# Optimization experiments

Measured on AMD Instinct MI355X. Metric: run time of the kernel, lower is better.

## Reference

```python
import jax, jax.numpy as jnp
import numpy as np

B, N, D = 2, 2048, 2048
H = 16
HD = D // H  # 128


def setup_inputs() -> dict:
    key = jax.random.key(0)
    k1, k2, k3 = jax.random.split(key, 3)
    x = jax.random.normal(k1, (B, N, D), dtype=jnp.float32)
    # Linear weights stored as [in, out] so y = x @ W matches torch's x @ W.T
    Wq = jax.random.normal(k2, (D, D), dtype=jnp.float32) * (D ** -0.5)
    Wo = jax.random.normal(k3, (D, D), dtype=jnp.float32) * (D ** -0.5)
    bo = jnp.zeros((D,), dtype=jnp.float32)
    return {"x": x, "Wq": Wq, "Wo": Wo, "bo": bo}


def reference(x, Wq, Wo, bo):
    # NOTE: source module (faithfully) projects q, k, v all with q_matrix.
    b, n, d = x.shape
    q = x @ Wq                                   # [B, N, D]
    qh = q.reshape(b, n, H, HD).transpose(0, 2, 1, 3)  # [B, H, N, HD]
    scores = jnp.einsum("bhnd,bhmd->bhnm", qh, qh) * (HD ** -0.5)  # [B,H,N,N]
    attn = jax.nn.softmax(scores, axis=-1)
    y = jnp.einsum("bhnm,bhmd->bhnd", attn, qh)  # [B, H, N, HD]
    y = y.transpose(0, 2, 1, 3).reshape(b, n, d)  # [B, N, D]
    return y @ Wo + bo
```

## Files before the change

### kernel.cpp

```cpp
#include <hip/hip_runtime.h>
#include <hip/hip_bf16.h>

#define BATCH 2
#define SEQ   2048
#define DIM   2048
#define NHEAD 16
#define HDIM  128

#define KSTRIDE 136
#define VSTRIDE 72
#define PSTRIDE 72

typedef __bf16 bf16;
typedef __attribute__((ext_vector_type(2))) __bf16 bf16x2;
typedef __attribute__((ext_vector_type(4))) __bf16 bf16x4;
typedef __attribute__((ext_vector_type(8))) __bf16 bf16x8;
typedef __attribute__((ext_vector_type(4))) float f32x4;

__device__ __forceinline__ void load_lds16(const bf16* g, bf16* l) {
    __builtin_amdgcn_global_load_lds((const __attribute__((address_space(1))) void*)g,
                                     (__attribute__((address_space(3))) void*)l, 16, 0, 0);
}

__device__ __forceinline__ float exp2_hw(float x) { return __builtin_amdgcn_exp2f(x); }

__global__ __launch_bounds__(256)
void prep_kernel(const float* __restrict__ x, bf16* __restrict__ xb,
                 const float* __restrict__ Wq, bf16* __restrict__ Wtq,
                 const float* __restrict__ Wo, bf16* __restrict__ Wto)
{
    __shared__ bf16 T[64 * 72];
    const int bid = blockIdx.x;
    if (bid < 4096) {
        const size_t i = ((size_t)bid * 256 + threadIdx.x) * 8;
        const float4 f0 = *(const float4*)(x + i);
        const float4 f1 = *(const float4*)(x + i + 4);
        *(bf16x8*)(xb + i) = (bf16x8){(bf16)f0.x, (bf16)f0.y, (bf16)f0.z, (bf16)f0.w,
                                      (bf16)f1.x, (bf16)f1.y, (bf16)f1.z, (bf16)f1.w};
        return;
    }
    int t = bid - 4096;
    const float* W  = (t < 1024) ? Wq : Wo;
    bf16*        Wt = (t < 1024) ? Wtq : Wto;
    t &= 1023;
    const int kb = (t >> 5) * 64, nb = (t & 31) * 64;

    const int a = threadIdx.x & 31;
    const int g = threadIdx.x >> 5;
    {
        const float* s0 = W + (size_t)(kb + 2 * a) * DIM + nb + g * 8;
        const float4 r0a = *(const float4*)(s0);
        const float4 r0b = *(const float4*)(s0 + 4);
        const float4 r1a = *(const float4*)(s0 + DIM);
        const float4 r1b = *(const float4*)(s0 + DIM + 4);
        float v0[8] = {r0a.x, r0a.y, r0a.z, r0a.w, r0b.x, r0b.y, r0b.z, r0b.w};
        float v1[8] = {r1a.x, r1a.y, r1a.z, r1a.w, r1b.x, r1b.y, r1b.z, r1b.w};
        #pragma unroll
        for (int i = 0; i < 8; ++i)
            *(bf16x2*)&T[(g * 8 + i) * 72 + 2 * a] = (bf16x2){(bf16)v0[i], (bf16)v1[i]};
    }
    __syncthreads();

    const int r  = threadIdx.x >> 2;
    const int k0 = (threadIdx.x & 3) * 16;
    bf16x8 o0 = *(const bf16x8*)&T[r * 72 + k0];
    bf16x8 o1 = *(const bf16x8*)&T[r * 72 + k0 + 8];
    *(bf16x8*)(Wt + (size_t)(nb + r) * DIM + kb + k0)     = o0;
    *(bf16x8*)(Wt + (size_t)(nb + r) * DIM + kb + k0 + 8) = o1;
}

template<bool OUT_F32_BIAS>
__global__ __launch_bounds__(256)
void gemm_bt(const bf16* __restrict__ A, const bf16* __restrict__ Bt,
             const float* __restrict__ bias, void* __restrict__ Cptr,
             int M, int N, int K)
{
    __shared__ bf16 As[2][128 * 32];
    __shared__ bf16 Bs[2][128 * 32];

    const int tid  = threadIdx.x;
    const int wave = tid >> 6;
    const int lane = tid & 63;
    const int quad = lane >> 4;
    const int l16  = lane & 15;
    const int wr   = (wave >> 1) * 64;
    const int wc   = (wave & 1) * 64;
    const int rowBase = blockIdx.y * 128;
    const int colBase = blockIdx.x * 128;

    const int srow = lane >> 2;
    const int scol = (lane & 3) * 8;
    const bf16* aBase = A  + (size_t)(rowBase + wave * 16 + srow) * K + scol;
    const bf16* bBase = Bt + (size_t)(colBase + wave * 16 + srow) * K + scol;

    f32x4 acc[4][4] = {};

    for (int k0 = 0; k0 < K; k0 += 64) {
        #pragma unroll
        for (int rh = 0; rh < 2; ++rh) {
            #pragma unroll
            for (int kh = 0; kh < 2; ++kh) {
                load_lds16(aBase + (size_t)rh * 64 * K + k0 + kh * 32,
                           (bf16*)As[kh] + (rh * 64 + wave * 16) * 32);
                load_lds16(bBase + (size_t)rh * 64 * K + k0 + kh * 32,
                           (bf16*)Bs[kh] + (rh * 64 + wave * 16) * 32);
            }
        }
        __syncthreads();

        #pragma unroll
        for (int ks = 0; ks < 2; ++ks) {
            bf16x8 a[4], b[4];
            #pragma unroll
            for (int i = 0; i < 4; ++i)
                a[i] = *(const bf16x8*)&As[ks][(wr + i * 16 + l16) * 32 + quad * 8];
            #pragma unroll
            for (int j = 0; j < 4; ++j)
                b[j] = *(const bf16x8*)&Bs[ks][(wc + j * 16 + l16) * 32 + quad * 8];
            #pragma unroll
            for (int i = 0; i < 4; ++i)
                #pragma unroll
                for (int j = 0; j < 4; ++j)
                    acc[i][j] = __builtin_amdgcn_mfma_f32_16x16x32_bf16(a[i], b[j], acc[i][j], 0, 0, 0);
        }
        __syncthreads();
    }

    #pragma unroll
    for (int i = 0; i < 4; ++i) {
        #pragma unroll
        for (int j = 0; j < 4; ++j) {
            #pragma unroll
            for (int r = 0; r < 4; ++r) {
                const int row = rowBase + wr + i * 16 + quad * 4 + r;
                const int col = colBase + wc + j * 16 + l16;
                const float v = acc[i][j][r];
                if (OUT_F32_BIAS) ((float*)Cptr)[(size_t)row * N + col] = v + bias[col];
                else              ((bf16*)Cptr)[(size_t)row * N + col] = (bf16)v;
            }
        }
    }
}

__global__ __launch_bounds__(256, 2)
void attn_kernel(const bf16* __restrict__ q, bf16* __restrict__ y)
{
    __shared__ bf16 Ks[64 * KSTRIDE];
    __shared__ bf16 Vt[HDIM * VSTRIDE];
    __shared__ bf16 Ps[128 * PSTRIDE];

    const int tid  = threadIdx.x;
    const int wave = tid >> 6;
    const int lane = tid & 63;
    const int quad = lane >> 4;
    const int l16  = lane & 15;

    const int p   = blockIdx.x;
    const int xcd = p & 7;
    const int pos = p >> 3;
    const int g   = xcd * 4 + (pos & 3);
    const int qt  = pos >> 2;
    const int h   = g & 15;
    const int bb  = g >> 4;

    const bf16* qb = q + (size_t)bb * SEQ * DIM + (size_t)h * HDIM;

    const float qs = 0.12752820031096662f;
    bf16x8 aq[2][4];
    #pragma unroll
    for (int nt = 0; nt < 2; ++nt) {
        #pragma unroll
        for (int ks = 0; ks < 4; ++ks) {
            const bf16* src = qb + (size_t)(qt * 128 + wave * 32 + nt * 16 + l16) * DIM + ks * 32 + quad * 8;
            bf16x8 v = *(const bf16x8*)src;
            bf16x8 o;
            #pragma unroll
            for (int e = 0; e < 8; ++e) o[e] = (bf16)((float)v[e] * qs);
            aq[nt][ks] = o;
        }
    }

    float lpart[2] = {0.f, 0.f};
    f32x4 yacc[2][8] = {};

    const int kr   = tid >> 2;
    const int koff = (tid & 3) * 32;
    const int sp   = tid & 31;
    const int ss   = tid >> 5;

    const bf16* srcK = qb + (size_t)kr * DIM + koff;
    const bf16* srcV = qb + (size_t)(2 * sp) * DIM + ss * 16;

    bf16x8 kreg[4], va[2], vb[2];
    #pragma unroll
    for (int c = 0; c < 4; ++c) kreg[c] = *(const bf16x8*)(srcK + c * 8);
    va[0] = *(const bf16x8*)(srcV + 0);
    va[1] = *(const bf16x8*)(srcV + 8);
    vb[0] = *(const bf16x8*)(srcV + DIM + 0);
    vb[1] = *(const bf16x8*)(srcV + DIM + 8);

    for (int kt = 0; kt < SEQ / 64; ++kt) {
        __syncthreads();

        #pragma unroll
        for (int c = 0; c < 4; ++c)
            *(bf16x8*)&Ks[kr * KSTRIDE + koff + c * 8] = kreg[c];
        #pragma unroll
        for (int c = 0; c < 2; ++c)
            #pragma unroll
            for (int e = 0; e < 8; ++e)
                *(bf16x2*)&Vt[(ss * 16 + c * 8 + e) * VSTRIDE + 2 * sp] = (bf16x2){va[c][e], vb[c][e]};

        if (kt + 1 < SEQ / 64) {
            const bf16* nK = srcK + (size_t)(kt + 1) * 64 * DIM;
            const bf16* nV = srcV + (size_t)(kt + 1) * 64 * DIM;
            #pragma unroll
            for (int c = 0; c < 4; ++c) kreg[c] = *(const bf16x8*)(nK + c * 8);
            va[0] = *(const bf16x8*)(nV + 0);
            va[1] = *(const bf16x8*)(nV + 8);
            vb[0] = *(const bf16x8*)(nV + DIM + 0);
            vb[1] = *(const bf16x8*)(nV + DIM + 8);
        }
        __syncthreads();

        #pragma unroll
        for (int mt = 0; mt < 4; ++mt) {
            bf16x8 ak[4];
            #pragma unroll
            for (int ks = 0; ks < 4; ++ks)
                ak[ks] = *(const bf16x8*)&Ks[(mt * 16 + l16) * KSTRIDE + ks * 32 + quad * 8];
            f32x4 s[2] = {};
            __builtin_amdgcn_s_setprio(1);
            #pragma unroll
            for (int ks = 0; ks < 4; ++ks)
                #pragma unroll
                for (int nt = 0; nt < 2; ++nt)
                    s[nt] = __builtin_amdgcn_mfma_f32_16x16x32_bf16(ak[ks], aq[nt][ks], s[nt], 0, 0, 0);
            __builtin_amdgcn_s_setprio(0);
            #pragma unroll
            for (int nt = 0; nt < 2; ++nt) {
                float p0 = exp2_hw(s[nt][0]);
                float p1 = exp2_hw(s[nt][1]);
                float p2 = exp2_hw(s[nt][2]);
                float p3 = exp2_hw(s[nt][3]);
                lpart[nt] += (p0 + p1) + (p2 + p3);
                *(bf16x4*)&Ps[(wave * 32 + nt * 16 + l16) * PSTRIDE + mt * 16 + quad * 4] =
                    (bf16x4){(bf16)p0, (bf16)p1, (bf16)p2, (bf16)p3};
            }
        }

        #pragma unroll
        for (int ks2 = 0; ks2 < 2; ++ks2) {
            bf16x8 ap[2];
            #pragma unroll
            for (int i = 0; i < 2; ++i)
                ap[i] = *(const bf16x8*)&Ps[(wave * 32 + i * 16 + l16) * PSTRIDE + ks2 * 32 + quad * 8];
            __builtin_amdgcn_s_setprio(1);
            #pragma unroll
            for (int n = 0; n < 8; ++n) {
                bf16x8 bv = *(const bf16x8*)&Vt[(n * 16 + l16) * VSTRIDE + ks2 * 32 + quad * 8];
                #pragma unroll
                for (int i = 0; i < 2; ++i)
                    yacc[i][n] = __builtin_amdgcn_mfma_f32_16x16x32_bf16(ap[i], bv, yacc[i][n], 0, 0, 0);
            }
            __builtin_amdgcn_s_setprio(0);
        }
    }

    float lfull[2];
    #pragma unroll
    for (int nt = 0; nt < 2; ++nt) {
        float l = lpart[nt];
        l += __shfl_xor(l, 16);
        l += __shfl_xor(l, 32);
        lfull[nt] = l;
    }

    bf16* yb = y + (size_t)bb * SEQ * DIM + (size_t)(qt * 128) * DIM + (size_t)h * HDIM;
    #pragma unroll
    for (int i = 0; i < 2; ++i) {
        #pragma unroll
        for (int r = 0; r < 4; ++r) {
            const float lv  = __shfl(lfull[i], (lane & 48) | (quad * 4 + r));
            const float inv = 1.f / lv;
            const int row = wave * 32 + i * 16 + quad * 4 + r;
            #pragma unroll
            for (int n = 0; n < 8; ++n)
                yb[(size_t)row * DIM + n * 16 + l16] = (bf16)(yacc[i][n][r] * inv);
        }
    }
}

extern "C" void kernel_launch(void* const* d_in, const int* in_sizes, int n_in,
                              void* d_out, int out_size, void* d_ws, size_t ws_size,
                              hipStream_t stream)
{
    const float* x  = (const float*)d_in[0];
    const float* Wq = (const float*)d_in[1];
    const float* Wo = (const float*)d_in[2];
    const float* bo = (const float*)d_in[3];
    float* out = (float*)d_out;

    const size_t NELEM = (size_t)BATCH * SEQ * DIM;
    bf16* qws = (bf16*)d_ws;
    bf16* yws = qws + NELEM;
    bf16* Wtq = yws;
    bf16* Wto = qws + 2 * NELEM;
    bf16* xb  = (bf16*)d_out;

    const int M = BATCH * SEQ;
    dim3 gg(DIM / 128, M / 128);

    prep_kernel<<<6144, 256, 0, stream>>>(x, xb, Wq, Wtq, Wo, Wto);
    gemm_bt<false><<<gg, 256, 0, stream>>>(xb, Wtq, nullptr, qws, M, DIM, DIM);
    attn_kernel<<<512, 256, 0, stream>>>(qws, yws);
    gemm_bt<true><<<gg, 256, 0, stream>>>(yws, Wto, bo, out, M, DIM, DIM);
}
```

Measured before the change: 274.4 us.

## Rewrite GEMM as 8-wave 128x256 tile with 4-stage LDS pipeline and swizzle

The bf16 GEMM kernel moves to 512 threads per block with a 128x256 output tile. Global-to-LDS loads run through a 4-slot ring buffer with manual vmcnt waits and raw barriers, and MFMA sections are raised to priority 1. LDS addresses are XOR-swizzled to avoid bank conflicts, and blocks are remapped so neighbouring blocks share B columns for L2 reuse. The goal is to hide global load latency behind the matrix math and cut the barrier stalls of the old double-buffered loop, at the cost of 96KB LDS per block and a hardcoded K=2048 step count.

Result: faster. 264.8 us (-3.5%).

```diff
diff --git a/kernel.cpp b/kernel.cpp
--- a/kernel.cpp
+++ b/kernel.cpp
@@ -69,62 +69,101 @@
     *(bf16x8*)(Wt + (size_t)(nb + r) * DIM + kb + k0 + 8) = o1;
 }
 
+#define GEMM_PHASE(S, VM, DO_STAGE)                                            \
+    {                                                                          \
+        const bf16* Aq = Ls + ((S) & 3) * 12288;                               \
+        const bf16* Bq = Aq + 4096;                                            \
+        bf16x8 a[4], b[4];                                                     \
+        _Pragma("unroll")                                                      \
+        for (int i = 0; i < 4; ++i) a[i] = *(const bf16x8*)(Aq + offA[i]);     \
+        _Pragma("unroll")                                                      \
+        for (int j = 0; j < 4; ++j) b[j] = *(const bf16x8*)(Bq + offB[j]);     \
+        if (DO_STAGE) {                                                        \
+            bf16* lb = Ls + (((S) + 3) & 3) * 12288 + wave * 512;              \
+            const int ko = ((S) + 3) * 32;                                     \
+            load_lds16(gA + ko, lb);                                           \
+            load_lds16(gB0 + ko, lb + 4096);                                   \
+            load_lds16(gB1 + ko, lb + 8192);                                   \
+        }                                                                      \
+        __builtin_amdgcn_s_barrier();                                          \
+        __builtin_amdgcn_s_setprio(1);                                         \
+        _Pragma("unroll")                                                      \
+        for (int i = 0; i < 4; ++i) {                                          \
+            _Pragma("unroll")                                                  \
+            for (int j = 0; j < 4; ++j)                                        \
+                acc[i][j] = __builtin_amdgcn_mfma_f32_16x16x32_bf16(a[i], b[j], acc[i][j], 0, 0, 0); \
+        }                                                                      \
+        __builtin_amdgcn_s_setprio(0);                                         \
+        if ((VM) == 6)      asm volatile("s_waitcnt vmcnt(6)" ::: "memory");   \
+        else if ((VM) == 3) asm volatile("s_waitcnt vmcnt(3)" ::: "memory");   \
+        else if ((VM) == 0) asm volatile("s_waitcnt vmcnt(0)" ::: "memory");   \
+        if ((VM) >= 0) {                                                       \
+            __builtin_amdgcn_s_barrier();                                      \
+            asm volatile("" ::: "memory");                                     \
+        }                                                                      \
+    }
+
 template<bool OUT_F32_BIAS>
-__global__ __launch_bounds__(256)
-void gemm_bt(const bf16* __restrict__ A, const bf16* __restrict__ Bt,
-             const float* __restrict__ bias, void* __restrict__ Cptr,
-             int M, int N, int K)
+__global__ __launch_bounds__(512, 2)
+void gemm_bt8(const bf16* __restrict__ A, const bf16* __restrict__ Bt,
+              const float* __restrict__ bias, void* __restrict__ Cptr,
+              int M, int N, int K)
 {
-    __shared__ bf16 As[2][128 * 32];
-    __shared__ bf16 Bs[2][128 * 32];
+    __shared__ bf16 Ls[4 * 12288];
 
     const int tid  = threadIdx.x;
     const int wave = tid >> 6;
     const int lane = tid & 63;
     const int quad = lane >> 4;
     const int l16  = lane & 15;
-    const int wr   = (wave >> 1) * 64;
-    const int wc   = (wave & 1) * 64;
-    const int rowBase = blockIdx.y * 128;
-    const int colBase = blockIdx.x * 128;
-
-    const int srow = lane >> 2;
-    const int scol = (lane & 3) * 8;
-    const bf16* aBase = A  + (size_t)(rowBase + wave * 16 + srow) * K + scol;
-    const bf16* bBase = Bt + (size_t)(colBase + wave * 16 + srow) * K + scol;
+    const int wr   = wave >> 2;
+    const int wc   = wave & 3;
+
+    const int cpx = gridDim.x >> 3;
+    const int logical = (blockIdx.x & 7) * cpx + (blockIdx.x >> 3);
+    const int rowBase = (logical >> 3) * 128;
+    const int colBase = (logical & 7) * 256;
+
+    int offA[4], offB[4];
+    #pragma unroll
+    for (int i = 0; i < 4; ++i) {
+        int e = (wr * 64 + i * 16 + l16) * 32 + quad * 8;
+        offA[i] = e ^ (((e >> 6) & 3) << 3);
+    }
+    #pragma unroll
+    for (int j = 0; j < 4; ++j) {
+        int e = (wc * 64 + j * 16 + l16) * 32 + quad * 8;
+        offB[j] = e ^ (((e >> 6) & 3) << 3);
+    }
+
+    const int oA  = wave * 512 + lane * 8;
+    const int eA  = oA ^ (((oA >> 6) & 3) << 3);
+    const bf16* gA  = A  + (size_t)(rowBase + (eA >> 5)) * K + (eA & 31);
+    const int oB0 = wave * 512 + lane * 8;
+    const int eB0 = oB0 ^ (((oB0 >> 6) & 3) << 3);
+    const bf16* gB0 = Bt + (size_t)(colBase + (eB0 >> 5)) * K + (eB0 & 31);
+    const int oB1 = 4096 + wave * 512 + lane * 8;
+    const int eB1 = oB1 ^ (((oB1 >> 6) & 3) << 3);
+    const bf16* gB1 = Bt + (size_t)(colBase + ((eB1 - 4096) >> 5) + 128) * K + (eB1 & 31);
 
     f32x4 acc[4][4] = {};
 
-    for (int k0 = 0; k0 < K; k0 += 64) {
-        #pragma unroll
-        for (int rh = 0; rh < 2; ++rh) {
-            #pragma unroll
-            for (int kh = 0; kh < 2; ++kh) {
-                load_lds16(aBase + (size_t)rh * 64 * K + k0 + kh * 32,
-                           (bf16*)As[kh] + (rh * 64 + wave * 16) * 32);
-                load_lds16(bBase + (size_t)rh * 64 * K + k0 + kh * 32,
-                           (bf16*)Bs[kh] + (rh * 64 + wave * 16) * 32);
-            }
-        }
-        __syncthreads();
-
-        #pragma unroll
-        for (int ks = 0; ks < 2; ++ks) {
-            bf16x8 a[4], b[4];
-            #pragma unroll
-            for (int i = 0; i < 4; ++i)
-                a[i] = *(const bf16x8*)&As[ks][(wr + i * 16 + l16) * 32 + quad * 8];
-            #pragma unroll
-            for (int j = 0; j < 4; ++j)
-                b[j] = *(const bf16x8*)&Bs[ks][(wc + j * 16 + l16) * 32 + quad * 8];
-            #pragma unroll
-            for (int i = 0; i < 4; ++i)
-                #pragma unroll
-                for (int j = 0; j < 4; ++j)
-                    acc[i][j] = __builtin_amdgcn_mfma_f32_16x16x32_bf16(a[i], b[j], acc[i][j], 0, 0, 0);
-        }
-        __syncthreads();
-    }
+    #pragma unroll
+    for (int s = 0; s < 3; ++s) {
+        bf16* lb = Ls + s * 12288 + wave * 512;
+        load_lds16(gA  + s * 32, lb);
+        load_lds16(gB0 + s * 32, lb + 4096);
+        load_lds16(gB1 + s * 32, lb + 8192);
+    }
+    asm volatile("s_waitcnt vmcnt(6)" ::: "memory");
+    __builtin_amdgcn_s_barrier();
+    asm volatile("" ::: "memory");
+
+    for (int s = 0; s < 61; ++s)
+        GEMM_PHASE(s, 6, true);
+    GEMM_PHASE(61, 3, false);
+    GEMM_PHASE(62, 0, false);
+    GEMM_PHASE(63, -1, false);
 
     #pragma unroll
     for (int i = 0; i < 4; ++i) {
@@ -132,8 +171,8 @@
         for (int j = 0; j < 4; ++j) {
             #pragma unroll
             for (int r = 0; r < 4; ++r) {
-                const int row = rowBase + wr + i * 16 + quad * 4 + r;
-                const int col = colBase + wc + j * 16 + l16;
+                const int row = rowBase + wr * 64 + i * 16 + quad * 4 + r;
+                const int col = colBase + wc * 64 + j * 16 + l16;
                 const float v = acc[i][j][r];
                 if (OUT_F32_BIAS) ((float*)Cptr)[(size_t)row * N + col] = v + bias[col];
                 else              ((bf16*)Cptr)[(size_t)row * N + col] = (bf16)v;
@@ -309,10 +348,9 @@
     bf16* xb  = (bf16*)d_out;
 
     const int M = BATCH * SEQ;
-    dim3 gg(DIM / 128, M / 128);
 
     prep_kernel<<<6144, 256, 0, stream>>>(x, xb, Wq, Wtq, Wo, Wto);
-    gemm_bt<false><<<gg, 256, 0, stream>>>(xb, Wtq, nullptr, qws, M, DIM, DIM);
+    gemm_bt8<false><<<256, 512, 0, stream>>>(xb, Wtq, nullptr, qws, M, DIM, DIM);
     attn_kernel<<<512, 256, 0, stream>>>(qws, yws);
-    gemm_bt<true><<<gg, 256, 0, stream>>>(yws, Wto, bo, out, M, DIM, DIM);
-}
+    gemm_bt8<true><<<256, 512, 0, stream>>>(yws, Wto, bo, out, M, DIM, DIM);
+}
```
